# Kernel tuning notes

Measured on AMD Instinct MI355X. Metric: run time of the kernel, lower is better.

The kernel has to match this reference:

```python
import jax, jax.numpy as jnp
import numpy as np

B, T, D, E, H = 4, 2048, 2048, 4, 8192  # H = 4*D
TOPK = 2
CAPACITY_FACTOR = 1


def setup_inputs() -> dict:
    key = jax.random.key(0)
    k0, k1, k2, k3 = jax.random.split(key, 4)
    x = jax.random.normal(k0, (B, T, D), dtype=jnp.float32)
    Wg = jax.random.normal(k1, (D, E), dtype=jnp.float32) * 0.02  # router gate weight
    bg = jnp.zeros((E,), dtype=jnp.float32)                        # router gate bias (nn.Linear default)
    W1 = jax.random.normal(k2, (E, D, H), dtype=jnp.float32) * (1.0 / np.sqrt(D))  # per-expert fc (no bias)
    W2 = jax.random.normal(k3, (E, H, D), dtype=jnp.float32) * (1.0 / np.sqrt(H))  # per-expert proj (no bias)
    return {"x": x, "Wg": Wg, "bg": bg, "W1": W1, "W2": W2}


def reference(x, Wg, bg, W1, W2):
    Bq, Tq, Dq = x.shape
    N = Bq * Tq
    capacity = int(N * CAPACITY_FACTOR / E)  # static python int

    flat_x = x.reshape(N, Dq)
    logits = flat_x @ Wg + bg                              # [N, E]
    top_vals, top_idx = jax.lax.top_k(logits, TOPK)        # [N, TOPK]
    sparse = jnp.full_like(logits, -jnp.inf)
    sparse = sparse.at[jnp.arange(N)[:, None], top_idx].set(top_vals)
    probs = jax.nn.softmax(sparse, axis=-1)                # zeros outside top-k

    out = jnp.zeros_like(flat_x)
    for i in range(E):  # small fixed expert count
        assigned = (top_idx == i).any(axis=-1)             # [N]
        score = jnp.where(assigned, probs[:, i], -jnp.inf)
        sel_p, sel_idx = jax.lax.top_k(score, capacity)    # capacity-limited, highest prob first
        p = jnp.where(jnp.isfinite(sel_p), sel_p, 0.0)[:, None]  # invalid slots contribute 0
        tok = flat_x[sel_idx]                              # [cap, D]
        h = jax.nn.gelu(tok @ W1[i], approximate=False)    # exact GELU like nn.GELU()
        y = (h @ W2[i]) * p                                # [cap, D]
        out = out.at[sel_idx].add(y)
    return out.reshape(Bq, Tq, Dq)
```

## Files before the change

### kernel.cpp

```cpp
#include <hip/hip_runtime.h>
#include <hip/hip_bf16.h>
#include <math.h>
#include <stdint.h>

#define N_TOK 8192
#define DMODEL 2048
#define NEXP 4
#define HDIM 8192
#define CAP 2048

typedef __attribute__((ext_vector_type(4))) float f32x4;
typedef __attribute__((ext_vector_type(8))) short s16x8;
typedef __attribute__((ext_vector_type(4))) unsigned short u16x4;

__device__ __forceinline__ unsigned short f2bf(float f) {
  __hip_bfloat16 h = __float2bfloat16(f);
  return __builtin_bit_cast(unsigned short, h);
}

__device__ __forceinline__ void gload_lds16(const void* g, void* l) {
  __builtin_amdgcn_global_load_lds(
      (const __attribute__((address_space(1))) unsigned int*)(uintptr_t)g,
      (__attribute__((address_space(3))) unsigned int*)(unsigned int)(uintptr_t)l,
      16, 0, 0);
}

__global__ __launch_bounds__(256) void router_kernel(
    const float* __restrict__ x, const float* __restrict__ Wg,
    const float* __restrict__ bg, unsigned long long* __restrict__ keys) {
  int token = blockIdx.x * 4 + (threadIdx.x >> 6);
  int lane = threadIdx.x & 63;
  const float* xr = x + (size_t)token * DMODEL;
  double a0 = 0, a1 = 0, a2 = 0, a3 = 0;
  for (int i = lane; i < DMODEL; i += 64) {
    float xv = xr[i];
    float4 w = ((const float4*)Wg)[i];
    a0 += (double)xv * (double)w.x;
    a1 += (double)xv * (double)w.y;
    a2 += (double)xv * (double)w.z;
    a3 += (double)xv * (double)w.w;
  }
  for (int off = 32; off > 0; off >>= 1) {
    a0 += __shfl_down(a0, off);
    a1 += __shfl_down(a1, off);
    a2 += __shfl_down(a2, off);
    a3 += __shfl_down(a3, off);
  }
  if (lane == 0) {
    float l[4] = {(float)(a0 + (double)bg[0]), (float)(a1 + (double)bg[1]),
                  (float)(a2 + (double)bg[2]), (float)(a3 + (double)bg[3])};
    int e1 = 0;
    for (int e = 1; e < 4; ++e) if (l[e] > l[e1]) e1 = e;
    int e2 = (e1 == 0) ? 1 : 0;
    for (int e = e2 + 1; e < 4; ++e) { if (e == e1) continue; if (l[e] > l[e2]) e2 = e; }
    float d = l[e2] - l[e1];
    float ex = expf(d);
    float z = 1.0f + ex;
    float p1 = 1.0f / z, p2 = ex / z;
    unsigned lo = 0xFFFFFFFFu - (unsigned)token;
    for (int e = 0; e < 4; ++e) {
      unsigned hi = (e == e1) ? __float_as_uint(p1) : (e == e2) ? __float_as_uint(p2) : 0u;
      keys[(size_t)e * N_TOK + token] = ((unsigned long long)hi << 32) | lo;
    }
  }
}

__global__ __launch_bounds__(256) void rank_select_kernel(
    const unsigned long long* __restrict__ keys, int* __restrict__ sel_idx,
    float* __restrict__ sel_p) {
  __shared__ unsigned long long kbuf[2048];
  const int e = blockIdx.y;
  const int i = blockIdx.x * 256 + threadIdx.x;
  const unsigned long long my = keys[(size_t)e * N_TOK + i];
  int rank = 0;
  for (int c = 0; c < N_TOK; c += 2048) {
    __syncthreads();
    for (int j = threadIdx.x; j < 2048; j += 256)
      kbuf[j] = keys[(size_t)e * N_TOK + c + j];
    __syncthreads();
#pragma unroll 8
    for (int j = 0; j < 2048; j += 2) {
      unsigned long long k0 = kbuf[j], k1 = kbuf[j + 1];
      rank += (k0 > my) + (k1 > my);
    }
  }
  if (rank < CAP) {
    sel_idx[e * CAP + rank] = i;
    sel_p[e * CAP + rank] = __uint_as_float((unsigned)(my >> 32));
  }
}

__global__ __launch_bounds__(256) void gather_kernel(
    const float* __restrict__ x, const int* __restrict__ sel_idx,
    unsigned short* __restrict__ tok) {
  int row = blockIdx.x;
  int t = sel_idx[row];
  const float4* src = (const float4*)(x + (size_t)t * DMODEL);
  u16x4* dst = (u16x4*)(tok + (size_t)row * DMODEL);
  for (int i = threadIdx.x; i < DMODEL / 4; i += blockDim.x) {
    float4 v = src[i];
    u16x4 w = {f2bf(v.x), f2bf(v.y), f2bf(v.z), f2bf(v.w)};
    dst[i] = w;
  }
}

__global__ __launch_bounds__(256) void transpose_convert_kernel(
    const float* __restrict__ W, unsigned short* __restrict__ WT, int K, int N) {
  __shared__ unsigned short tile[64][68];
  const size_t eoff = (size_t)blockIdx.z * (size_t)K * N;
  const float* Wp = W + eoff;
  unsigned short* Tp = WT + eoff;
  const int n0 = blockIdx.x * 64, k0 = blockIdx.y * 64;
  const int tid = threadIdx.x;
  const int nn4 = tid & 15, kk = tid >> 4;
#pragma unroll
  for (int p = 0; p < 4; ++p) {
    int k = kk + p * 16;
    float4 v = *(const float4*)&Wp[(size_t)(k0 + k) * N + n0 + nn4 * 4];
    tile[nn4 * 4 + 0][k] = f2bf(v.x);
    tile[nn4 * 4 + 1][k] = f2bf(v.y);
    tile[nn4 * 4 + 2][k] = f2bf(v.z);
    tile[nn4 * 4 + 3][k] = f2bf(v.w);
  }
  __syncthreads();
  const int nw = tid >> 4, cw = (tid & 15) * 4;
#pragma unroll
  for (int p = 0; p < 4; ++p) {
    int n = nw + p * 16;
    u16x4 v = *(const u16x4*)&tile[n][cw];
    *(u16x4*)&Tp[(size_t)(n0 + n) * K + k0 + cw] = v;
  }
}

template <int EPI>
__global__ __launch_bounds__(512) void gemm_kernel(
    const unsigned short* __restrict__ A, const unsigned short* __restrict__ Bt,
    void* __restrict__ C, const int* __restrict__ sel_idx, const float* __restrict__ sel_p,
    int M, int N, int K, size_t b_stride) {
  __shared__ unsigned short sh[65536];
  const int tid = threadIdx.x;
  const int lane = tid & 63;
  const int w = tid >> 6;
  const int wm = w >> 2, wn = w & 3;

  const int nwg = gridDim.x * gridDim.y;
  const int cpx = nwg >> 3;
  int linear = blockIdx.y * gridDim.x + blockIdx.x;
  linear = (linear & 7) * cpx + (linear >> 3);
  const int bx = linear & (gridDim.x - 1);
  const int by = linear >> __builtin_ctz(gridDim.x);
  const int m0 = by * 256, n0 = bx * 256;
  const unsigned short* Bp = Bt + (size_t)(m0 >> 11) * b_stride;

  f32x4 acc[8][4];
#pragma unroll
  for (int i = 0; i < 8; ++i)
#pragma unroll
    for (int j = 0; j < 4; ++j) acc[i][j] = (f32x4){0.f, 0.f, 0.f, 0.f};

  const int srow = w * 16 + (lane >> 2);
  const int schunk = ((lane & 3) ^ ((lane >> 3) & 3)) * 8;
  const unsigned short* gA = A + (size_t)(m0 + srow) * K + schunk;
  const unsigned short* gB = Bp + (size_t)(n0 + srow) * K + schunk;
  const int ldsSt = w * 512;

#define STA(slot, j) do { \
    gload_lds16(gA + (size_t)(j) * 32, &sh[(slot) * 8192 + ldsSt]); \
    gload_lds16(gA + (size_t)128 * K + (size_t)(j) * 32, &sh[(slot) * 8192 + 4096 + ldsSt]); \
  } while (0)
#define STB(slot, j) do { \
    gload_lds16(gB + (size_t)(j) * 32, &sh[32768 + (slot) * 8192 + ldsSt]); \
    gload_lds16(gB + (size_t)128 * K + (size_t)(j) * 32, &sh[32768 + (slot) * 8192 + 4096 + ldsSt]); \
  } while (0)

  const int arow = wm * 128 + (lane & 15);
  const int brow = wn * 64 + (lane & 15);
  const int koff = (((lane >> 4) ^ ((lane >> 1) & 3)) << 3);

  STA(0, 0); STB(0, 0);
  STA(1, 1); STB(1, 1);
  STA(2, 2); STB(2, 2);
  asm volatile("s_waitcnt vmcnt(8)" ::: "memory");
  __builtin_amdgcn_s_barrier();

  const int NS = K >> 5;
  for (int j = 0; j < NS; ++j) {
    const unsigned short* sa = &sh[(j & 3) * 8192];
    const unsigned short* sb = &sh[32768 + (j & 3) * 8192];
    const bool pf = (j + 3) < NS;
    const int psl = (j + 3) & 3;
    s16x8 av[4], bv[4];
#pragma unroll
    for (int nf = 0; nf < 4; ++nf)
      bv[nf] = *(const s16x8*)&sb[(brow + nf * 16) * 32 + koff];
#pragma unroll
    for (int mf = 0; mf < 4; ++mf)
      av[mf] = *(const s16x8*)&sa[(arow + mf * 16) * 32 + koff];
    if (pf) STA(psl, j + 3);
    __builtin_amdgcn_s_barrier();
    asm volatile("s_waitcnt lgkmcnt(0)" ::: "memory");
    __builtin_amdgcn_sched_barrier(0);
    __builtin_amdgcn_s_setprio(1);
#pragma unroll
    for (int mf = 0; mf < 4; ++mf)
#pragma unroll
      for (int nf = 0; nf < 4; ++nf)
        acc[mf][nf] = __builtin_amdgcn_mfma_f32_16x16x32_bf16(av[mf], bv[nf], acc[mf][nf], 0, 0, 0);
    __builtin_amdgcn_s_setprio(0);
    __builtin_amdgcn_s_barrier();
#pragma unroll
    for (int mf = 0; mf < 4; ++mf)
      av[mf] = *(const s16x8*)&sa[(arow + 64 + mf * 16) * 32 + koff];
    if (pf) STB(psl, j + 3);
    if (pf)                   asm volatile("s_waitcnt vmcnt(8)" ::: "memory");
    else if ((j + 2) < NS)    asm volatile("s_waitcnt vmcnt(4)" ::: "memory");
    else                      asm volatile("s_waitcnt vmcnt(0)" ::: "memory");
    __builtin_amdgcn_s_barrier();
    asm volatile("s_waitcnt lgkmcnt(0)" ::: "memory");
    __builtin_amdgcn_sched_barrier(0);
    __builtin_amdgcn_s_setprio(1);
#pragma unroll
    for (int mf = 0; mf < 4; ++mf)
#pragma unroll
      for (int nf = 0; nf < 4; ++nf)
        acc[4 + mf][nf] = __builtin_amdgcn_mfma_f32_16x16x32_bf16(av[mf], bv[nf], acc[4 + mf][nf], 0, 0, 0);
    __builtin_amdgcn_s_setprio(0);
    __builtin_amdgcn_s_barrier();
  }
#undef STA
#undef STB

  if (EPI == 0) {
    unsigned short* Hc = (unsigned short*)C;
#pragma unroll
    for (int mf = 0; mf < 8; ++mf) {
      int rowb = m0 + wm * 128 + mf * 16 + ((lane >> 4) << 2);
#pragma unroll
      for (int nf = 0; nf < 4; ++nf) {
        int col = n0 + wn * 64 + nf * 16 + (lane & 15);
#pragma unroll
        for (int r = 0; r < 4; ++r) {
          float v = acc[mf][nf][r];
          float g = 0.5f * v * (1.0f + erff(v * 0.70710678118654752f));
          Hc[(size_t)(rowb + r) * N + col] = f2bf(g);
        }
      }
    }
  } else {
    float* O = (float*)C;
#pragma unroll
    for (int mf = 0; mf < 8; ++mf) {
      int rowb = m0 + wm * 128 + mf * 16 + ((lane >> 4) << 2);
      int tk[4];
      float pv[4];
#pragma unroll
      for (int r = 0; r < 4; ++r) { tk[r] = sel_idx[rowb + r]; pv[r] = sel_p[rowb + r]; }
#pragma unroll
      for (int nf = 0; nf < 4; ++nf) {
        int col = n0 + wn * 64 + nf * 16 + (lane & 15);
#pragma unroll
        for (int r = 0; r < 4; ++r)
          atomicAdd(&O[(size_t)tk[r] * DMODEL + col], acc[mf][nf][r] * pv[r]);
      }
    }
  }
}

extern "C" void kernel_launch(void* const* d_in, const int* in_sizes, int n_in,
                              void* d_out, int out_size, void* d_ws, size_t ws_size,
                              hipStream_t stream) {
  const float* x  = (const float*)d_in[0];
  const float* Wg = (const float*)d_in[1];
  const float* bg = (const float*)d_in[2];
  const float* W1 = (const float*)d_in[3];
  const float* W2 = (const float*)d_in[4];
  float* out = (float*)d_out;

  char* ws = (char*)d_ws;
  unsigned long long* keys = (unsigned long long*)ws;
  int*   sel_idx = (int*)(ws + 262144);
  float* sel_p   = (float*)(ws + 262144 + 32768);
  unsigned short* tok = (unsigned short*)(ws + 327680);
  const size_t tok_b = (size_t)N_TOK * DMODEL * 2;
  const size_t h_b   = (size_t)N_TOK * HDIM * 2;
  const size_t w_b   = (size_t)NEXP * DMODEL * HDIM * 2;
  const size_t base  = 327680 + tok_b;

  hipMemsetAsync(d_out, 0, (size_t)out_size * sizeof(float), stream);
  router_kernel<<<N_TOK / 4, 256, 0, stream>>>(x, Wg, bg, keys);
  rank_select_kernel<<<dim3(N_TOK / 256, NEXP), 256, 0, stream>>>(keys, sel_idx, sel_p);
  gather_kernel<<<NEXP * CAP, 256, 0, stream>>>(x, sel_idx, tok);

  if (ws_size >= base + h_b + 2 * w_b) {
    unsigned short* h   = (unsigned short*)(ws + base);
    unsigned short* W1T = (unsigned short*)(ws + base + h_b);
    unsigned short* W2T = (unsigned short*)(ws + base + h_b + w_b);
    transpose_convert_kernel<<<dim3(HDIM / 64, DMODEL / 64, NEXP), 256, 0, stream>>>(
        W1, W1T, DMODEL, HDIM);
    transpose_convert_kernel<<<dim3(DMODEL / 64, HDIM / 64, NEXP), 256, 0, stream>>>(
        W2, W2T, HDIM, DMODEL);
    gemm_kernel<0><<<dim3(HDIM / 256, N_TOK / 256), 512, 0, stream>>>(
        tok, W1T, h, nullptr, nullptr, N_TOK, HDIM, DMODEL, (size_t)DMODEL * HDIM);
    gemm_kernel<1><<<dim3(DMODEL / 256, N_TOK / 256), 512, 0, stream>>>(
        h, W2T, out, sel_idx, sel_p, N_TOK, DMODEL, HDIM, (size_t)DMODEL * HDIM);
  } else {
    unsigned short* h    = (unsigned short*)(ws + base);
    unsigned short* wbuf = (unsigned short*)(ws + base + (size_t)CAP * HDIM * 2);
    for (int e = 0; e < NEXP; ++e) {
      transpose_convert_kernel<<<dim3(HDIM / 64, DMODEL / 64, 1), 256, 0, stream>>>(
          W1 + (size_t)e * DMODEL * HDIM, wbuf, DMODEL, HDIM);
      gemm_kernel<0><<<dim3(HDIM / 256, CAP / 256), 512, 0, stream>>>(
          tok + (size_t)e * CAP * DMODEL, wbuf, h, nullptr, nullptr, CAP, HDIM, DMODEL, 0);
      transpose_convert_kernel<<<dim3(DMODEL / 64, HDIM / 64, 1), 256, 0, stream>>>(
          W2 + (size_t)e * HDIM * DMODEL, wbuf, HDIM, DMODEL);
      gemm_kernel<1><<<dim3(DMODEL / 256, CAP / 256), 512, 0, stream>>>(
          h, wbuf, out, sel_idx + e * CAP, sel_p + e * CAP, CAP, DMODEL, HDIM, 0);
    }
  }
}
```

Before: 894.5 us.

## Double-buffer LDS fragment registers to overlap ds_reads with MFMA in GEMM loop

Restructures the GEMM main loop to unroll by two and keep two register sets of A/B fragments (even and odd). The LDS reads for the next k-step are issued before the MFMAs of the current step, so LDS latency overlaps with matrix math. This also halves the barriers per step, merges the A and B global-to-LDS staging into one macro, and sets launch_bounds to one block per CU. The extra fragment registers raise VGPR pressure, which the occupancy hint is meant to allow.

After: 955.7 us. 6.8% more time.

```diff
diff --git a/kernel.cpp b/kernel.cpp
--- a/kernel.cpp
+++ b/kernel.cpp
@@ -133,7 +133,7 @@
 }
 
 template <int EPI>
-__global__ __launch_bounds__(512) void gemm_kernel(
+__global__ __launch_bounds__(512, 1) void gemm_kernel(
     const unsigned short* __restrict__ A, const unsigned short* __restrict__ Bt,
     void* __restrict__ C, const int* __restrict__ sel_idx, const float* __restrict__ sel_p,
     int M, int N, int K, size_t b_stride) {
@@ -164,11 +164,9 @@
   const unsigned short* gB = Bp + (size_t)(n0 + srow) * K + schunk;
   const int ldsSt = w * 512;
 
-#define STA(slot, j) do { \
+#define STAGE(slot, j) do { \
     gload_lds16(gA + (size_t)(j) * 32, &sh[(slot) * 8192 + ldsSt]); \
     gload_lds16(gA + (size_t)128 * K + (size_t)(j) * 32, &sh[(slot) * 8192 + 4096 + ldsSt]); \
-  } while (0)
-#define STB(slot, j) do { \
     gload_lds16(gB + (size_t)(j) * 32, &sh[32768 + (slot) * 8192 + ldsSt]); \
     gload_lds16(gB + (size_t)128 * K + (size_t)(j) * 32, &sh[32768 + (slot) * 8192 + 4096 + ldsSt]); \
   } while (0)
@@ -177,58 +175,72 @@
   const int brow = wn * 64 + (lane & 15);
   const int koff = (((lane >> 4) ^ ((lane >> 1) & 3)) << 3);
 
-  STA(0, 0); STB(0, 0);
-  STA(1, 1); STB(1, 1);
-  STA(2, 2); STB(2, 2);
-  asm volatile("s_waitcnt vmcnt(8)" ::: "memory");
-  __builtin_amdgcn_s_barrier();
+#define DSREAD(slot, AV, BV) do { \
+    const unsigned short* sa_ = &sh[(slot) * 8192]; \
+    const unsigned short* sb_ = &sh[32768 + (slot) * 8192]; \
+    _Pragma("unroll") \
+    for (int nf = 0; nf < 4; ++nf) BV[nf] = *(const s16x8*)&sb_[(brow + nf * 16) * 32 + koff]; \
+    _Pragma("unroll") \
+    for (int mf = 0; mf < 8; ++mf) AV[mf] = *(const s16x8*)&sa_[(arow + mf * 16) * 32 + koff]; \
+  } while (0)
+
+#define MFMA32(AV, BV) do { \
+    __builtin_amdgcn_s_setprio(1); \
+    _Pragma("unroll") \
+    for (int mf = 0; mf < 8; ++mf) \
+      _Pragma("unroll") \
+      for (int nf = 0; nf < 4; ++nf) \
+        acc[mf][nf] = __builtin_amdgcn_mfma_f32_16x16x32_bf16(AV[mf], BV[nf], acc[mf][nf], 0, 0, 0); \
+    __builtin_amdgcn_s_setprio(0); \
+  } while (0)
+
+#define VMW(n) asm volatile("s_waitcnt vmcnt(" #n ")" ::: "memory")
+#define BARF() do { __builtin_amdgcn_s_barrier(); asm volatile("" ::: "memory"); } while (0)
+
+  STAGE(0, 0); STAGE(1, 1); STAGE(2, 2);
+  VMW(8);
+  BARF();
+  s16x8 Aev[8], Bev[4], Aod[8], Bod[4];
+  DSREAD(0, Aev, Bev);
 
   const int NS = K >> 5;
-  for (int j = 0; j < NS; ++j) {
-    const unsigned short* sa = &sh[(j & 3) * 8192];
-    const unsigned short* sb = &sh[32768 + (j & 3) * 8192];
-    const bool pf = (j + 3) < NS;
-    const int psl = (j + 3) & 3;
-    s16x8 av[4], bv[4];
-#pragma unroll
-    for (int nf = 0; nf < 4; ++nf)
-      bv[nf] = *(const s16x8*)&sb[(brow + nf * 16) * 32 + koff];
-#pragma unroll
-    for (int mf = 0; mf < 4; ++mf)
-      av[mf] = *(const s16x8*)&sa[(arow + mf * 16) * 32 + koff];
-    if (pf) STA(psl, j + 3);
-    __builtin_amdgcn_s_barrier();
-    asm volatile("s_waitcnt lgkmcnt(0)" ::: "memory");
-    __builtin_amdgcn_sched_barrier(0);
-    __builtin_amdgcn_s_setprio(1);
-#pragma unroll
-    for (int mf = 0; mf < 4; ++mf)
-#pragma unroll
-      for (int nf = 0; nf < 4; ++nf)
-        acc[mf][nf] = __builtin_amdgcn_mfma_f32_16x16x32_bf16(av[mf], bv[nf], acc[mf][nf], 0, 0, 0);
-    __builtin_amdgcn_s_setprio(0);
-    __builtin_amdgcn_s_barrier();
-#pragma unroll
-    for (int mf = 0; mf < 4; ++mf)
-      av[mf] = *(const s16x8*)&sa[(arow + 64 + mf * 16) * 32 + koff];
-    if (pf) STB(psl, j + 3);
-    if (pf)                   asm volatile("s_waitcnt vmcnt(8)" ::: "memory");
-    else if ((j + 2) < NS)    asm volatile("s_waitcnt vmcnt(4)" ::: "memory");
-    else                      asm volatile("s_waitcnt vmcnt(0)" ::: "memory");
-    __builtin_amdgcn_s_barrier();
-    asm volatile("s_waitcnt lgkmcnt(0)" ::: "memory");
-    __builtin_amdgcn_sched_barrier(0);
-    __builtin_amdgcn_s_setprio(1);
-#pragma unroll
-    for (int mf = 0; mf < 4; ++mf)
-#pragma unroll
-      for (int nf = 0; nf < 4; ++nf)
-        acc[4 + mf][nf] = __builtin_amdgcn_mfma_f32_16x16x32_bf16(av[mf], bv[nf], acc[4 + mf][nf], 0, 0, 0);
-    __builtin_amdgcn_s_setprio(0);
-    __builtin_amdgcn_s_barrier();
-  }
-#undef STA
-#undef STB
+  for (int j = 0; j < NS; j += 2) {
+    {
+      if (j + 3 < NS) STAGE((j + 3) & 3, j + 3);
+      const int newer = (NS - 1 < j + 3 ? NS - 1 : j + 3) - (j + 1);
+      if (newer >= 2) VMW(8);
+      else if (newer == 1) VMW(4);
+      else VMW(0);
+      BARF();
+      DSREAD((j + 1) & 3, Aod, Bod);
+      __builtin_amdgcn_sched_barrier(0);
+      MFMA32(Aev, Bev);
+      BARF();
+    }
+    {
+      const int jj = j + 1;
+      if (jj + 3 < NS) STAGE((jj + 3) & 3, jj + 3);
+      const bool rd = (jj + 1) < NS;
+      if (rd) {
+        const int newer = (NS - 1 < jj + 3 ? NS - 1 : jj + 3) - (jj + 1);
+        if (newer >= 2) VMW(8);
+        else if (newer == 1) VMW(4);
+        else VMW(0);
+      }
+      BARF();
+      if (rd) {
+        DSREAD((jj + 1) & 3, Aev, Bev);
+        __builtin_amdgcn_sched_barrier(0);
+      }
+      MFMA32(Aod, Bod);
+      BARF();
+    }
+  }
+#undef STAGE
+#undef DSREAD
+#undef MFMA32
+#undef VMW
+#undef BARF
 
   if (EPI == 0) {
     unsigned short* Hc = (unsigned short*)C;
```
